# Kernel tuning notes

Measured on AMD Instinct MI355X. Metric: run time of the kernel, lower is better.

Reference implementation:

```python
import jax, jax.numpy as jnp
import numpy as np

DIM = 1024
SRC_DIM = 1152
NUM_HEADS = 16
HEAD_DIM = DIM // NUM_HEADS  # 64
ROPE_BASE = 10000.0


def rope_tables(seq_len, head_dim):
    # matches RotaryPositionEmbedding: inv_freq over even indices, emb = cat([freqs, freqs])
    inv_freq = 1.0 / (ROPE_BASE ** (jnp.arange(0, head_dim, 2, dtype=jnp.float32) / head_dim))
    t = jnp.arange(seq_len, dtype=jnp.float32)
    freqs = t[:, None] * inv_freq[None, :]          # (L, D/2)
    emb = jnp.concatenate([freqs, freqs], axis=-1)  # (L, D)
    return jnp.cos(emb), jnp.sin(emb)


def rotate_half(x):
    # interleaved rotation as in the torch code
    x1 = x[..., ::2]
    x2 = x[..., 1::2]
    return jnp.stack((-x2, x1), axis=-1).reshape(x.shape)


def apply_rope(t, cos, sin):
    # t: (B, H, L, D); cos/sin: (L, D)
    return t * cos[None, None] + rotate_half(t) * sin[None, None]


def setup_inputs() -> dict:
    key = jax.random.key(0)
    ks = jax.random.split(key, 10)
    B, T, K = 2, 2048, 2048
    s_q = 1.0 / np.sqrt(DIM)
    s_kv = 1.0 / np.sqrt(SRC_DIM)
    return {
        "x": jax.random.normal(ks[0], (B, T, DIM), jnp.float32),
        "context": jax.random.normal(ks[1], (B, K, SRC_DIM), jnp.float32),
        "Wq": jax.random.normal(ks[2], (DIM, DIM), jnp.float32) * s_q,
        "bq": jnp.zeros((DIM,), jnp.float32),
        "Wk": jax.random.normal(ks[3], (DIM, SRC_DIM), jnp.float32) * s_kv,
        "bk": jnp.zeros((DIM,), jnp.float32),
        "Wv": jax.random.normal(ks[4], (DIM, SRC_DIM), jnp.float32) * s_kv,
        "bv": jnp.zeros((DIM,), jnp.float32),
        "Wo": jax.random.normal(ks[5], (DIM, DIM), jnp.float32) * s_q,
        "bo": jnp.zeros((DIM,), jnp.float32),
    }


def reference(x, context, Wq, bq, Wk, bk, Wv, bv, Wo, bo):
    B, T, C = x.shape
    K = context.shape[1]
    H, D = NUM_HEADS, HEAD_DIM

    q = x @ Wq.T + bq                 # (B, T, C)
    k = context @ Wk.T + bk           # (B, K, C)
    v = context @ Wv.T + bv           # (B, K, C)

    q = q.reshape(B, T, H, D).transpose(0, 2, 1, 3)  # (B, H, T, D)
    k = k.reshape(B, K, H, D).transpose(0, 2, 1, 3)  # (B, H, K, D)
    v = v.reshape(B, K, H, D).transpose(0, 2, 1, 3)

    cos_q, sin_q = rope_tables(T, D)
    cos_k, sin_k = rope_tables(K, D)
    q = apply_rope(q, cos_q, sin_q)
    k = apply_rope(k, cos_k, sin_k)

    scale = 1.0 / np.sqrt(D).astype(np.float32)
    scores = jnp.einsum('bhtd,bhkd->bhtk', q, k) * scale  # (B, H, T, K)
    weights = jax.nn.softmax(scores, axis=-1)
    out = jnp.einsum('bhtk,bhkd->bhtd', weights, v)        # (B, H, T, D)
    out = out.transpose(0, 2, 1, 3).reshape(B, T, C)
    return out @ Wo.T + bo
```

## Files before the change

kernel.cpp:

```cpp
#include <hip/hip_runtime.h>
#include <hip/hip_bf16.h>
#include <stdint.h>

typedef unsigned short u16;
typedef __attribute__((ext_vector_type(8))) short bf16x8;
typedef __attribute__((ext_vector_type(8))) unsigned short u16x8;
typedef __attribute__((ext_vector_type(4))) float f32x4;

#define BM 128
#define BN 128
#define BK 32
#define QBK 64
#define QSCALE 0.18033688f

__device__ __forceinline__ u16 f2bf(float f) {
    union { float f; uint32_t u; } v; v.f = f;
    uint32_t r = v.u + 0x7FFFu + ((v.u >> 16) & 1u);
    return (u16)(r >> 16);
}

__device__ __forceinline__ uint32_t cvt_pk_bf16(float lo, float hi) {
    uint32_t r;
    asm("v_cvt_pk_bf16_f32 %0, %1, %2" : "=v"(r) : "v"(lo), "v"(hi));
    return r;
}

__device__ __forceinline__ float fexp2(float x) {
    float r;
    asm volatile("v_exp_f32 %0, %1\n\ts_nop 0" : "=v"(r) : "v"(x));
    return r;
}

__device__ __forceinline__ void gload_lds16(const void* g, void* l) {
    __builtin_amdgcn_global_load_lds(
        (const __attribute__((address_space(1))) void*)(g),
        (__attribute__((address_space(3))) void*)(l),
        16, 0, 0);
}

__global__ void prep_kernel(const float* __restrict__ x, const float* __restrict__ ctx,
                            const float* __restrict__ Wq, const float* __restrict__ Wk,
                            const float* __restrict__ Wv, const float* __restrict__ Wo,
                            u16* __restrict__ xb, u16* __restrict__ cb,
                            u16* __restrict__ wqb, u16* __restrict__ wkb,
                            u16* __restrict__ wvb, u16* __restrict__ wob,
                            float2* __restrict__ cs) {
    int t = blockIdx.x * 256 + threadIdx.x;
    if (t < 3342336) {
        const float* src; u16* dst; int base;
        if      (t < 1048576) { src = x;   dst = xb;  base = 0; }
        else if (t < 2228224) { src = ctx; dst = cb;  base = 1048576; }
        else if (t < 2490368) { src = Wq;  dst = wqb; base = 2228224; }
        else if (t < 2785280) { src = Wk;  dst = wkb; base = 2490368; }
        else if (t < 3080192) { src = Wv;  dst = wvb; base = 2785280; }
        else                  { src = Wo;  dst = wob; base = 3080192; }
        int i = (t - base) * 4;
        float4 v = *reinterpret_cast<const float4*>(src + i);
        ushort4 o = { f2bf(v.x), f2bf(v.y), f2bf(v.z), f2bf(v.w) };
        *reinterpret_cast<ushort4*>(dst + i) = o;
    } else {
        int idx = t - 3342336;
        int tt = idx >> 5, j = idx & 31;
        float invf = 1.0f / powf(10000.0f, (float)(2 * j) / 64.0f);
        float ang = (float)tt * invf;
        cs[idx] = make_float2(cosf(ang), sinf(ang));
    }
}

__global__ __launch_bounds__(256, 3)
void qkv_gemm(const u16* __restrict__ xb, const u16* __restrict__ cb,
              const u16* __restrict__ wqb, const u16* __restrict__ wkb,
              const u16* __restrict__ wvb,
              const float* __restrict__ bq, const float* __restrict__ bk,
              const float* __restrict__ bv,
              u16* __restrict__ qo, u16* __restrict__ ko, u16* __restrict__ vo,
              const float2* __restrict__ cs)
{
    __shared__ __align__(16) u16 As[BM * QBK];
    __shared__ __align__(16) u16 Bs[BN * QBK];
    const int bid = blockIdx.x;
    const int wg = (bid & 7) * 96 + (bid >> 3);
    const int seg = wg >> 8, inner = wg & 255;
    const u16* A; const u16* Bm; const float* bias; u16* C;
    int N, K, mbase, nbase, rope, brow;
    float oscale;
    if (seg == 0)      { A = xb;  Bm = wqb; bias = bq; C = qo; N = 1024; K = 1024; rope = 1; brow = 0; oscale = QSCALE; nbase = (inner & 7) * BN;  mbase = (inner >> 3) * BM; }
    else if (seg == 1) { A = cb;  Bm = wkb; bias = bk; C = ko; N = 1024; K = 1152; rope = 1; brow = 0; oscale = 1.0f;   nbase = (inner & 7) * BN;  mbase = (inner >> 3) * BM; }
    else               { A = wvb; Bm = cb;  bias = bv; C = vo; N = 4096; K = 1152; rope = 0; brow = 1; oscale = 1.0f;   nbase = (inner & 31) * BN; mbase = (inner >> 5) * BM; }

    const int tid = threadIdx.x;
    const int wid = tid >> 6, lane = tid & 63;
    const int wr = wid >> 1, wc = wid & 1;
    const int l15 = lane & 15, l4 = lane >> 4;
    const int r8 = lane >> 3;
    const int cp = lane & 7;
    const int cl = cp ^ r8;

    f32x4 acc[4][4];
#pragma unroll
    for (int i = 0; i < 4; i++)
#pragma unroll
        for (int j = 0; j < 4; j++) acc[i][j] = (f32x4){0.f, 0.f, 0.f, 0.f};

    for (int k0 = 0; k0 < K; k0 += QBK) {
#pragma unroll
        for (int q = 0; q < 4; ++q) {
            int sg = wid * 4 + q;
            int row = sg * 8 + r8;
            gload_lds16(A  + (size_t)(mbase + row) * K + k0 + cl * 8, (void*)(As + sg * 512));
            gload_lds16(Bm + (size_t)(nbase + row) * K + k0 + cl * 8, (void*)(Bs + sg * 512));
        }
        __syncthreads();
        bf16x8 af[2][4], bfv[2][4];
#pragma unroll
        for (int kk = 0; kk < 2; kk++) {
#pragma unroll
            for (int i = 0; i < 4; i++) {
                int r = wr * 64 + i * 16 + l15;
                af[kk][i] = *(const bf16x8*)(As + r * 64 + (((kk * 4 + l4) ^ (r & 7)) * 8));
            }
#pragma unroll
            for (int j = 0; j < 4; j++) {
                int r = wc * 64 + j * 16 + l15;
                bfv[kk][j] = *(const bf16x8*)(Bs + r * 64 + (((kk * 4 + l4) ^ (r & 7)) * 8));
            }
        }
        __builtin_amdgcn_s_setprio(1);
#pragma unroll
        for (int kk = 0; kk < 2; kk++)
#pragma unroll
            for (int i = 0; i < 4; i++)
#pragma unroll
                for (int j = 0; j < 4; j++)
                    acc[i][j] = __builtin_amdgcn_mfma_f32_16x16x32_bf16(af[kk][i], bfv[kk][j], acc[i][j], 0, 0, 0);
        __builtin_amdgcn_s_setprio(0);
        __syncthreads();
    }

#pragma unroll
    for (int i = 0; i < 4; i++) {
#pragma unroll
        for (int j = 0; j < 4; j++) {
#pragma unroll
            for (int r = 0; r < 4; r++) {
                int row = mbase + wr * 64 + i * 16 + l4 * 4 + r;
                int col = nbase + wc * 64 + j * 16 + l15;
                float v = acc[i][j][r] + (brow ? bias[row] : bias[col]);
                if (rope) {
                    float part = __shfl_xor(v, 1);
                    float2 c2 = cs[(row & 2047) * 32 + (col & 31)];
                    v = v * c2.x + ((col & 1) ? part * c2.y : -part * c2.y);
                    v *= oscale;
                }
                C[(size_t)row * N + col] = f2bf(v);
            }
        }
    }
}

__global__ __launch_bounds__(256, 2)
void gemm_out(const u16* __restrict__ A, const u16* __restrict__ B,
              const float* __restrict__ bias, float* __restrict__ C,
              int M, int N, int K)
{
    __shared__ __align__(16) u16 As[2][BM * BK];
    __shared__ __align__(16) u16 Bs[2][64 * BK];
    const int tid = threadIdx.x;
    const int wid = tid >> 6, lane = tid & 63;
    const int wr = wid >> 1, wc = wid & 1;
    const int l15 = lane & 15, l4 = lane >> 4;
    const int mbase = blockIdx.y * BM, nbase = blockIdx.x * 64;
    const int srow = lane >> 2;
    const int scol = (lane & 3) * 8;
    const int nk = K >> 5;

    f32x4 acc[4][2];
#pragma unroll
    for (int i = 0; i < 4; i++)
#pragma unroll
        for (int j = 0; j < 2; j++) acc[i][j] = (f32x4){0.f, 0.f, 0.f, 0.f};

    auto stage = [&](int bs, int k0) {
#pragma unroll
        for (int q = 0; q < 2; ++q) {
            int seg = wid * 2 + q;
            int row = seg * 16 + srow;
            gload_lds16(A + (size_t)(mbase + row) * K + k0 + scol, (void*)(&As[bs][seg * 512]));
        }
        {
            int row = wid * 16 + srow;
            gload_lds16(B + (size_t)(nbase + row) * K + k0 + scol, (void*)(&Bs[bs][wid * 512]));
        }
    };

    stage(0, 0);
    __syncthreads();
    int buf = 0;
    for (int ks = 0; ks < nk; ++ks) {
        if (ks + 1 < nk) stage(buf ^ 1, (ks + 1) * BK);
        bf16x8 af[4], bfv[2];
#pragma unroll
        for (int i = 0; i < 4; i++)
            af[i] = *(const bf16x8*)(&As[buf][(wr * 64 + i * 16 + l15) * BK + l4 * 8]);
#pragma unroll
        for (int j = 0; j < 2; j++)
            bfv[j] = *(const bf16x8*)(&Bs[buf][(wc * 32 + j * 16 + l15) * BK + l4 * 8]);
#pragma unroll
        for (int i = 0; i < 4; i++)
#pragma unroll
            for (int j = 0; j < 2; j++)
                acc[i][j] = __builtin_amdgcn_mfma_f32_16x16x32_bf16(af[i], bfv[j], acc[i][j], 0, 0, 0);
        __syncthreads();
        buf ^= 1;
    }

#pragma unroll
    for (int i = 0; i < 4; i++)
#pragma unroll
        for (int j = 0; j < 2; j++)
#pragma unroll
            for (int r = 0; r < 4; r++) {
                int row = mbase + wr * 64 + i * 16 + l4 * 4 + r;
                int col = nbase + wc * 32 + j * 16 + l15;
                C[(size_t)row * N + col] = acc[i][j][r] + bias[col];
            }
}

__device__ __forceinline__ int invrow(int R) {
    return 32 * (R >> 5) + 8 * ((R >> 2) & 3) + 4 * ((R >> 4) & 1) + (R & 3);
}

__global__ __launch_bounds__(256, 4)
void attn_kernel(const u16* __restrict__ Qb, const u16* __restrict__ Kb,
                 const u16* __restrict__ VT, u16* __restrict__ Ob)
{
    const int qt = blockIdx.x;
    const int bh = blockIdx.y;
    const int b = bh >> 4, h = bh & 15;
    __shared__ __align__(16) u16 Ks[2][4096];
    __shared__ __align__(16) u16 Vs[2][4096];
    const int tid = threadIdx.x, wv = tid >> 6, lane = tid & 63;
    const int l15 = lane & 15, l4 = lane >> 4;

    const int r8 = lane >> 3;
    const int cp = lane & 7;
    const int cl = cp ^ r8;
    const int L0 = 2 * wv, L1 = 2 * wv + 1;
    const int RK0 = L0 * 8 + r8, RK1 = L1 * 8 + r8;
    const u16* ksrc0 = Kb + (size_t)(b * 2048 + invrow(RK0)) * 1024 + h * 64 + cl * 8;
    const u16* ksrc1 = Kb + (size_t)(b * 2048 + invrow(RK1)) * 1024 + h * 64 + cl * 8;
    const u16* vsrc0 = VT + (size_t)(h * 64 + RK0) * 4096 + b * 2048 + cl * 8;
    const u16* vsrc1 = VT + (size_t)(h * 64 + RK1) * 4096 + b * 2048 + cl * 8;

    const u16* qrow = Qb + (size_t)(b * 2048 + qt * 64 + wv * 16 + l15) * 1024 + h * 64;
    bf16x8 qf0 = *(const bf16x8*)(qrow + l4 * 8);
    bf16x8 qf1 = *(const bf16x8*)(qrow + 32 + l4 * 8);

    const int swz = l15 & 7;
    const int q0o = (l4 ^ swz) * 8;
    const int q1o = ((4 + l4) ^ swz) * 8;

    f32x4 accO[4];
    float denom = 0.f;
#pragma unroll
    for (int i = 0; i < 4; i++) accO[i] = (f32x4){0.f, 0.f, 0.f, 0.f};

    auto stageK = [&](int bs, int kt) {
        gload_lds16(ksrc0 + (size_t)kt * 65536, (void*)&Ks[bs][L0 * 512]);
        gload_lds16(ksrc1 + (size_t)kt * 65536, (void*)&Ks[bs][L1 * 512]);
    };
    auto stageV = [&](int bs, int kt) {
        gload_lds16(vsrc0 + kt * 64, (void*)&Vs[bs][L0 * 512]);
        gload_lds16(vsrc1 + kt * 64, (void*)&Vs[bs][L1 * 512]);
    };

    stageK(0, 0);
    __syncthreads();

    f32x4 sA[4], sB[4];

    auto finish_tile = [&](f32x4 (&sold)[4], int vbuf) {
        float p[4][4];
        float rs = 0.f;
#pragma unroll
        for (int j = 0; j < 4; j++)
#pragma unroll
            for (int r = 0; r < 4; r++) {
                p[j][r] = fexp2(sold[j][r]);
                rs += p[j][r];
            }
        rs += __shfl_xor(rs, 16);
        rs += __shfl_xor(rs, 32);
        denom += rs;
        union { uint32_t u[4]; bf16x8 v; } B0u, B1u;
        B0u.u[0] = cvt_pk_bf16(p[0][0], p[0][1]);
        B0u.u[1] = cvt_pk_bf16(p[0][2], p[0][3]);
        B0u.u[2] = cvt_pk_bf16(p[1][0], p[1][1]);
        B0u.u[3] = cvt_pk_bf16(p[1][2], p[1][3]);
        B1u.u[0] = cvt_pk_bf16(p[2][0], p[2][1]);
        B1u.u[1] = cvt_pk_bf16(p[2][2], p[2][3]);
        B1u.u[2] = cvt_pk_bf16(p[3][0], p[3][1]);
        B1u.u[3] = cvt_pk_bf16(p[3][2], p[3][3]);
        __builtin_amdgcn_s_setprio(1);
#pragma unroll
        for (int i = 0; i < 4; i++) {
            const u16* vp = &Vs[vbuf][(i * 16 + l15) * 64];
            bf16x8 v0 = *(const bf16x8*)(vp + q0o);
            bf16x8 v1 = *(const bf16x8*)(vp + q1o);
            accO[i] = __builtin_amdgcn_mfma_f32_16x16x32_bf16(v0, B0u.v, accO[i], 0, 0, 0);
            accO[i] = __builtin_amdgcn_mfma_f32_16x16x32_bf16(v1, B1u.v, accO[i], 0, 0, 0);
        }
        __builtin_amdgcn_s_setprio(0);
    };

    auto body = [&](int kt, f32x4 (&snew)[4], f32x4 (&sold)[4]) {
        const int kb = kt & 1;
#pragma unroll
        for (int j = 0; j < 4; j++) snew[j] = (f32x4){0.f, 0.f, 0.f, 0.f};
        __builtin_amdgcn_s_setprio(1);
#pragma unroll
        for (int j = 0; j < 4; j++) {
            const u16* rp = &Ks[kb][(j * 16 + l15) * 64];
            bf16x8 a0 = *(const bf16x8*)(rp + q0o);
            bf16x8 a1 = *(const bf16x8*)(rp + q1o);
            snew[j] = __builtin_amdgcn_mfma_f32_16x16x32_bf16(a0, qf0, snew[j], 0, 0, 0);
            snew[j] = __builtin_amdgcn_mfma_f32_16x16x32_bf16(a1, qf1, snew[j], 0, 0, 0);
        }
        __builtin_amdgcn_s_setprio(0);
        if (kt < 31) stageK(kb ^ 1, kt + 1);
        stageV(kb ^ 1, kt);
        if (kt > 0) finish_tile(sold, kb);
        __syncthreads();
    };

    for (int kt2 = 0; kt2 < 32; kt2 += 2) {
        body(kt2, sA, sB);
        body(kt2 + 1, sB, sA);
    }
    finish_tile(sB, 0);

    float rd = 1.0f / denom;
    u16* orow = Ob + (size_t)(b * 2048 + qt * 64 + wv * 16 + l15) * 1024 + h * 64;
#pragma unroll
    for (int i = 0; i < 4; i++) {
        uint2 st;
        st.x = cvt_pk_bf16(accO[i][0] * rd, accO[i][1] * rd);
        st.y = cvt_pk_bf16(accO[i][2] * rd, accO[i][3] * rd);
        *(uint2*)(orow + i * 16 + l4 * 4) = st;
    }
}

extern "C" void kernel_launch(void* const* d_in, const int* in_sizes, int n_in,
                              void* d_out, int out_size, void* d_ws, size_t ws_size,
                              hipStream_t stream) {
    const float* x   = (const float*)d_in[0];
    const float* ctx = (const float*)d_in[1];
    const float* Wq  = (const float*)d_in[2];
    const float* bq  = (const float*)d_in[3];
    const float* Wk  = (const float*)d_in[4];
    const float* bk  = (const float*)d_in[5];
    const float* Wv  = (const float*)d_in[6];
    const float* bv  = (const float*)d_in[7];
    const float* Wo  = (const float*)d_in[8];
    const float* bo  = (const float*)d_in[9];
    float* out = (float*)d_out;

    char* ws = (char*)d_ws;
    size_t off = 0;
    auto alloc = [&](size_t bytes) { void* p = ws + off; off += (bytes + 255) & ~255ULL; return p; };
    u16* x_bf  = (u16*)alloc(4096ULL * 1024 * 2);
    u16* c_bf  = (u16*)alloc(4096ULL * 1152 * 2);
    u16* wq_bf = (u16*)alloc(1024ULL * 1024 * 2);
    u16* wk_bf = (u16*)alloc(1024ULL * 1152 * 2);
    u16* wv_bf = (u16*)alloc(1024ULL * 1152 * 2);
    u16* wo_bf = (u16*)alloc(1024ULL * 1024 * 2);
    float2* cs = (float2*)alloc(2048ULL * 32 * 8);
    u16* q_bf  = (u16*)alloc(4096ULL * 1024 * 2);
    u16* k_bf  = (u16*)alloc(4096ULL * 1024 * 2);
    u16* vT    = (u16*)alloc(1024ULL * 4096 * 2);
    u16* a_bf  = (u16*)alloc(4096ULL * 1024 * 2);

    prep_kernel<<<13312, 256, 0, stream>>>(x, ctx, Wq, Wk, Wv, Wo,
                                           x_bf, c_bf, wq_bf, wk_bf, wv_bf, wo_bf, cs);
    qkv_gemm<<<768, 256, 0, stream>>>(x_bf, c_bf, wq_bf, wk_bf, wv_bf,
                                      bq, bk, bv, q_bf, k_bf, vT, cs);
    attn_kernel<<<dim3(32, 32), 256, 0, stream>>>(q_bf, k_bf, vT, a_bf);
    gemm_out<<<dim3(16, 32), 256, 0, stream>>>(a_bf, wo_bf, bo, out, 4096, 1024, 1024);
}
```

Baseline: 135.0 us.

## Widen attention blocks to 8 waves and use swizzled single-buffer K=64 output GEMM

The attention kernel now runs 512 threads per block covering 128 query rows. Each K/V tile is loaded once and shared by twice as many waves, and each wave stages one row group instead of two. The output projection GEMM drops double-buffered K=32 staging for a single-buffered K=64 tile with an XOR-swizzled LDS layout and raised MFMA priority, meant to cut bank conflicts and barrier count. In exchange it loses overlap between global loads and compute in that GEMM, and halves the attention grid, which may reduce occupancy.

```diff
diff --git a/kernel.cpp b/kernel.cpp
--- a/kernel.cpp
+++ b/kernel.cpp
@@ -163,16 +163,16 @@
               const float* __restrict__ bias, float* __restrict__ C,
               int M, int N, int K)
 {
-    __shared__ __align__(16) u16 As[2][BM * BK];
-    __shared__ __align__(16) u16 Bs[2][64 * BK];
+    __shared__ __align__(16) u16 As[BM * QBK];
+    __shared__ __align__(16) u16 Bs[64 * QBK];
     const int tid = threadIdx.x;
     const int wid = tid >> 6, lane = tid & 63;
     const int wr = wid >> 1, wc = wid & 1;
     const int l15 = lane & 15, l4 = lane >> 4;
     const int mbase = blockIdx.y * BM, nbase = blockIdx.x * 64;
-    const int srow = lane >> 2;
-    const int scol = (lane & 3) * 8;
-    const int nk = K >> 5;
+    const int r8 = lane >> 3;
+    const int cp = lane & 7;
+    const int cl = cp ^ r8;
 
     f32x4 acc[4][2];
 #pragma unroll
@@ -180,38 +180,47 @@
 #pragma unroll
         for (int j = 0; j < 2; j++) acc[i][j] = (f32x4){0.f, 0.f, 0.f, 0.f};
 
-    auto stage = [&](int bs, int k0) {
+    for (int k0 = 0; k0 < K; k0 += QBK) {
+#pragma unroll
+        for (int q = 0; q < 4; ++q) {
+            int sg = wid * 4 + q;
+            int row = sg * 8 + r8;
+            gload_lds16(A + (size_t)(mbase + row) * K + k0 + cl * 8, (void*)(As + sg * 512));
+        }
+        {
+            int sg = wid * 2 + (lane >> 5);
+        }
 #pragma unroll
         for (int q = 0; q < 2; ++q) {
-            int seg = wid * 2 + q;
-            int row = seg * 16 + srow;
-            gload_lds16(A + (size_t)(mbase + row) * K + k0 + scol, (void*)(&As[bs][seg * 512]));
-        }
-        {
-            int row = wid * 16 + srow;
-            gload_lds16(B + (size_t)(nbase + row) * K + k0 + scol, (void*)(&Bs[bs][wid * 512]));
-        }
-    };
-
-    stage(0, 0);
-    __syncthreads();
-    int buf = 0;
-    for (int ks = 0; ks < nk; ++ks) {
-        if (ks + 1 < nk) stage(buf ^ 1, (ks + 1) * BK);
-        bf16x8 af[4], bfv[2];
-#pragma unroll
-        for (int i = 0; i < 4; i++)
-            af[i] = *(const bf16x8*)(&As[buf][(wr * 64 + i * 16 + l15) * BK + l4 * 8]);
-#pragma unroll
-        for (int j = 0; j < 2; j++)
-            bfv[j] = *(const bf16x8*)(&Bs[buf][(wc * 32 + j * 16 + l15) * BK + l4 * 8]);
-#pragma unroll
-        for (int i = 0; i < 4; i++)
-#pragma unroll
-            for (int j = 0; j < 2; j++)
-                acc[i][j] = __builtin_amdgcn_mfma_f32_16x16x32_bf16(af[i], bfv[j], acc[i][j], 0, 0, 0);
-        __syncthreads();
-        buf ^= 1;
+            int sg = wid * 2 + q;
+            int row = sg * 8 + r8;
+            gload_lds16(B + (size_t)(nbase + row) * K + k0 + cl * 8, (void*)(Bs + sg * 512));
+        }
+        __syncthreads();
+        bf16x8 af[2][4], bfv[2][2];
+#pragma unroll
+        for (int kk = 0; kk < 2; kk++) {
+#pragma unroll
+            for (int i = 0; i < 4; i++) {
+                int r = wr * 64 + i * 16 + l15;
+                af[kk][i] = *(const bf16x8*)(As + r * 64 + (((kk * 4 + l4) ^ (r & 7)) * 8));
+            }
+#pragma unroll
+            for (int j = 0; j < 2; j++) {
+                int r = wc * 32 + j * 16 + l15;
+                bfv[kk][j] = *(const bf16x8*)(Bs + r * 64 + (((kk * 4 + l4) ^ (r & 7)) * 8));
+            }
+        }
+        __builtin_amdgcn_s_setprio(1);
+#pragma unroll
+        for (int kk = 0; kk < 2; kk++)
+#pragma unroll
+            for (int i = 0; i < 4; i++)
+#pragma unroll
+                for (int j = 0; j < 2; j++)
+                    acc[i][j] = __builtin_amdgcn_mfma_f32_16x16x32_bf16(af[kk][i], bfv[kk][j], acc[i][j], 0, 0, 0);
+        __builtin_amdgcn_s_setprio(0);
+        __syncthreads();
     }
 
 #pragma unroll
@@ -230,7 +239,7 @@
     return 32 * (R >> 5) + 8 * ((R >> 2) & 3) + 4 * ((R >> 4) & 1) + (R & 3);
 }
 
-__global__ __launch_bounds__(256, 4)
+__global__ __launch_bounds__(512, 4)
 void attn_kernel(const u16* __restrict__ Qb, const u16* __restrict__ Kb,
                  const u16* __restrict__ VT, u16* __restrict__ Ob)
 {
@@ -245,14 +254,11 @@
     const int r8 = lane >> 3;
     const int cp = lane & 7;
     const int cl = cp ^ r8;
-    const int L0 = 2 * wv, L1 = 2 * wv + 1;
-    const int RK0 = L0 * 8 + r8, RK1 = L1 * 8 + r8;
-    const u16* ksrc0 = Kb + (size_t)(b * 2048 + invrow(RK0)) * 1024 + h * 64 + cl * 8;
-    const u16* ksrc1 = Kb + (size_t)(b * 2048 + invrow(RK1)) * 1024 + h * 64 + cl * 8;
-    const u16* vsrc0 = VT + (size_t)(h * 64 + RK0) * 4096 + b * 2048 + cl * 8;
-    const u16* vsrc1 = VT + (size_t)(h * 64 + RK1) * 4096 + b * 2048 + cl * 8;
-
-    const u16* qrow = Qb + (size_t)(b * 2048 + qt * 64 + wv * 16 + l15) * 1024 + h * 64;
+    const int RK = wv * 8 + r8;
+    const u16* ksrc = Kb + (size_t)(b * 2048 + invrow(RK)) * 1024 + h * 64 + cl * 8;
+    const u16* vsrc = VT + (size_t)(h * 64 + RK) * 4096 + b * 2048 + cl * 8;
+
+    const u16* qrow = Qb + (size_t)(b * 2048 + qt * 128 + wv * 16 + l15) * 1024 + h * 64;
     bf16x8 qf0 = *(const bf16x8*)(qrow + l4 * 8);
     bf16x8 qf1 = *(const bf16x8*)(qrow + 32 + l4 * 8);
 
@@ -266,12 +272,10 @@
     for (int i = 0; i < 4; i++) accO[i] = (f32x4){0.f, 0.f, 0.f, 0.f};
 
     auto stageK = [&](int bs, int kt) {
-        gload_lds16(ksrc0 + (size_t)kt * 65536, (void*)&Ks[bs][L0 * 512]);
-        gload_lds16(ksrc1 + (size_t)kt * 65536, (void*)&Ks[bs][L1 * 512]);
+        gload_lds16(ksrc + (size_t)kt * 65536, (void*)&Ks[bs][wv * 512]);
     };
     auto stageV = [&](int bs, int kt) {
-        gload_lds16(vsrc0 + kt * 64, (void*)&Vs[bs][L0 * 512]);
-        gload_lds16(vsrc1 + kt * 64, (void*)&Vs[bs][L1 * 512]);
+        gload_lds16(vsrc + kt * 64, (void*)&Vs[bs][wv * 512]);
     };
 
     stageK(0, 0);
@@ -340,7 +344,7 @@
     finish_tile(sB, 0);
 
     float rd = 1.0f / denom;
-    u16* orow = Ob + (size_t)(b * 2048 + qt * 64 + wv * 16 + l15) * 1024 + h * 64;
+    u16* orow = Ob + (size_t)(b * 2048 + qt * 128 + wv * 16 + l15) * 1024 + h * 64;
 #pragma unroll
     for (int i = 0; i < 4; i++) {
         uint2 st;
@@ -384,6 +388,6 @@
                                            x_bf, c_bf, wq_bf, wk_bf, wv_bf, wo_bf, cs);
     qkv_gemm<<<768, 256, 0, stream>>>(x_bf, c_bf, wq_bf, wk_bf, wv_bf,
                                       bq, bk, bv, q_bf, k_bf, vT, cs);
-    attn_kernel<<<dim3(32, 32), 256, 0, stream>>>(q_bf, k_bf, vT, a_bf);
+    attn_kernel<<<dim3(16, 32), 512, 0, stream>>>(q_bf, k_bf, vT, a_bf);
     gemm_out<<<dim3(16, 32), 256, 0, stream>>>(a_bf, wo_bf, bo, out, 4096, 1024, 1024);
 }
```

Result: faster. 125.9 us (-6.8%).
